# Optimization experiments

Hardware: AMD Instinct MI355X
Metric: run time of the kernel (lower is better)

## Reference

```python
import jax, jax.numpy as jnp
import numpy as np

N_NODES = 50000
N_EDGES = 600000
D = 128


def setup_inputs() -> dict:
    key = jax.random.key(0)
    k = jax.random.split(key, 6)
    x = jax.random.normal(k[0], (N_NODES, D), dtype=jnp.float32)
    edge_src = jax.random.randint(k[1], (N_EDGES,), 0, N_NODES, dtype=jnp.int64 if jax.config.jax_enable_x64 else jnp.int32)
    edge_dst = jax.random.randint(k[2], (N_EDGES,), 0, N_NODES, dtype=jnp.int64 if jax.config.jax_enable_x64 else jnp.int32)
    # message MLP: [h_src ; h_dst] (2D) -> D, update MLP: [h ; agg] (2D) -> D
    scale = 1.0 / np.sqrt(2 * D)
    W1 = jax.random.normal(k[3], (2 * D, D), dtype=jnp.float32) * scale
    b1 = jnp.zeros((D,), dtype=jnp.float32)
    W2 = jax.random.normal(k[4], (2 * D, D), dtype=jnp.float32) * scale
    b2 = jnp.zeros((D,), dtype=jnp.float32)
    return {"x": x, "edge_src": edge_src, "edge_dst": edge_dst,
            "W1": W1, "b1": b1, "W2": W2, "b2": b2}


def reference(x, edge_src, edge_dst, W1, b1, W2, b2):
    # gather endpoint features per edge: [E, 2D]
    pair = jnp.concatenate([x[edge_src], x[edge_dst]], axis=-1)
    # per-edge message MLP: [E, D]
    msg = jax.nn.relu(pair @ W1 + b1)
    # scatter-aggregate (sum) messages into destination nodes: [N, D]
    agg = jax.ops.segment_sum(msg, edge_dst, num_segments=N_NODES)
    # node update MLP with residual: [N, D]
    upd = jax.nn.relu(jnp.concatenate([x, agg], axis=-1) @ W2 + b2)
    return x + upd
```

## Files before the change

### kernel.cpp

```cpp
#include <hip/hip_runtime.h>
#include <stdint.h>


typedef __attribute__((ext_vector_type(8))) short short8;
typedef __attribute__((ext_vector_type(4))) float floatx4;

#define D 128
#define CAP 96

static __device__ __forceinline__ unsigned short f2bf(float f) {
    union { float f; unsigned int u; } v; v.f = f;
    unsigned int r = (v.u + 0x7fffu + ((v.u >> 16) & 1u)) >> 16;
    return (unsigned short)r;
}
static __device__ __forceinline__ float bflo(unsigned int u) {
    union { unsigned int u; float f; } v; v.u = u << 16; return v.f;
}
static __device__ __forceinline__ float bfhi(unsigned int u) {
    union { unsigned int u; float f; } v; v.u = u & 0xffff0000u; return v.f;
}

__global__ void k_pre(const float* __restrict__ W1, const float* __restrict__ W2,
                      unsigned short* __restrict__ w1f, unsigned short* __restrict__ w2f,
                      int* __restrict__ cnt, int N) {
    int gid = blockIdx.x * blockDim.x + threadIdx.x;
    if (gid < (N >> 2)) ((int4*)cnt)[gid] = make_int4(0, 0, 0, 0);
    if (gid < 32768) {
        int tid = gid;
        int j = tid & 7, lane = (tid >> 3) & 63, ct = (tid >> 9) & 15, kk = tid >> 13;
        int k = kk * 32 + (lane >> 4) * 8 + j;
        int c = ((ct >> 2) << 6) + ((lane & 15) << 2) + (ct & 3);
        float v = (c < 128) ? W1[k * 128 + c] : W1[(128 + k) * 128 + (c - 128)];
        w1f[tid] = f2bf(v);
    } else {
        int tid = gid - 32768;
        int j = tid & 7, lane = (tid >> 3) & 63, ct = (tid >> 9) & 7, kk = tid >> 12;
        int k = kk * 32 + (lane >> 4) * 8 + j;
        int c = ((ct >> 1) << 5) + ((lane & 15) << 1) + (ct & 1);
        w2f[tid] = f2bf(W2[k * 128 + c]);
    }
}

__global__ __launch_bounds__(256, 4) void k_fat1(
    const float* __restrict__ x,
    const unsigned short* __restrict__ w1f,
    const float* __restrict__ b1,
    unsigned short* __restrict__ Ys,
    unsigned short* __restrict__ Yd,
    const int* __restrict__ esrc,
    const int* __restrict__ edst,
    int* __restrict__ cnt,
    int* __restrict__ slot,
    int N, int nTiles, int nb1, int E)
{
    const int tid = threadIdx.x;
    if ((int)blockIdx.x >= nb1) {
        const int hthreads = (gridDim.x - nb1) * 256;
        const int hid = (blockIdx.x - nb1) * 256 + tid;
        const int E4 = E >> 2;
        for (int i = hid; i < E4; i += hthreads) {
            int4 s4 = ((const int4*)esrc)[i];
            int4 d4 = ((const int4*)edst)[i];
            int p;
            p = atomicAdd(&cnt[d4.x], 1); if (p < CAP) slot[d4.x * CAP + p] = s4.x;
            p = atomicAdd(&cnt[d4.y], 1); if (p < CAP) slot[d4.y * CAP + p] = s4.y;
            p = atomicAdd(&cnt[d4.z], 1); if (p < CAP) slot[d4.z * CAP + p] = s4.z;
            p = atomicAdd(&cnt[d4.w], 1); if (p < CAP) slot[d4.w * CAP + p] = s4.w;
        }
        for (int i = (E4 << 2) + hid; i < E; i += hthreads) {
            int p = atomicAdd(&cnt[edst[i]], 1);
            if (p < CAP) slot[edst[i] * CAP + p] = esrc[i];
        }
        return;
    }
    const int w = tid >> 6, lane = tid & 63;
    const int quad = lane >> 4, col = lane & 15;

    short8 wf[4][4];
#pragma unroll
    for (int kk = 0; kk < 4; kk++)
#pragma unroll
        for (int j = 0; j < 4; j++)
            wf[kk][j] = ((const short8*)w1f)[(kk * 16 + w * 4 + j) * 64 + lane];
    float4 bias = make_float4(0.f, 0.f, 0.f, 0.f);
    if (w >= 2) bias = *(const float4*)(b1 + (w - 2) * 64 + col * 4);
    unsigned short* Yhalf = (w < 2) ? Ys : Yd;
    const int cb = (w & 1) * 64;

    for (int t = blockIdx.x; t < nTiles; t += nb1) {
        const int n0 = t * 16;
        const int nr = n0 + col;
        const float* xrow = x + (long)nr * D;
        float4 f[8];
#pragma unroll
        for (int kk = 0; kk < 4; kk++) {
            f[kk * 2]     = *(const float4*)(xrow + kk * 32 + quad * 8);
            f[kk * 2 + 1] = *(const float4*)(xrow + kk * 32 + quad * 8 + 4);
        }
        floatx4 acc[4];
#pragma unroll
        for (int j = 0; j < 4; j++)
#pragma unroll
            for (int q = 0; q < 4; q++) acc[j][q] = 0.f;
#pragma unroll
        for (int kk = 0; kk < 4; kk++) {
            union { short8 s; unsigned int u[4]; } au;
            asm("v_cvt_pk_bf16_f32 %0, %1, %2" : "=v"(au.u[0]) : "v"(f[kk*2].x),   "v"(f[kk*2].y));
            asm("v_cvt_pk_bf16_f32 %0, %1, %2" : "=v"(au.u[1]) : "v"(f[kk*2].z),   "v"(f[kk*2].w));
            asm("v_cvt_pk_bf16_f32 %0, %1, %2" : "=v"(au.u[2]) : "v"(f[kk*2+1].x), "v"(f[kk*2+1].y));
            asm("v_cvt_pk_bf16_f32 %0, %1, %2" : "=v"(au.u[3]) : "v"(f[kk*2+1].z), "v"(f[kk*2+1].w));
#pragma unroll
            for (int j = 0; j < 4; j++)
                acc[j] = __builtin_amdgcn_mfma_f32_16x16x32_bf16(au.s, wf[kk][j], acc[j], 0, 0, 0);
        }
#pragma unroll
        for (int r = 0; r < 4; r++) {
            int n = n0 + quad * 4 + r;
            ushort4 o;
            o.x = f2bf(acc[0][r] + bias.x);
            o.y = f2bf(acc[1][r] + bias.y);
            o.z = f2bf(acc[2][r] + bias.z);
            o.w = f2bf(acc[3][r] + bias.w);
            *(ushort4*)(Yhalf + (long)n * D + cb + col * 4) = o;
        }
    }
}

__global__ __launch_bounds__(256) void k_agg(
    const unsigned short* __restrict__ Ys,
    const unsigned short* __restrict__ Yd,
    const int* __restrict__ cnt,
    const int* __restrict__ slot,
    unsigned short* __restrict__ aggb, int N)
{
    int wv = blockIdx.x * 4 + (threadIdx.x >> 6);
    if (wv >= N) return;
    int lane = threadIdx.x & 63;
    int deg = cnt[wv]; if (deg > CAP) deg = CAP;
    const int* sl = slot + wv * CAP;
    unsigned int ydu = *(const unsigned int*)(Yd + (long)wv * D + lane * 2);
    float yd0 = bflo(ydu), yd1 = bfhi(ydu);
    float a0 = 0.f, a1 = 0.f;
    const unsigned short* ysl = Ys + lane * 2;
    int e = 0;
    for (; e + 8 <= deg; e += 8) {
        int s[8]; unsigned int u[8];
#pragma unroll
        for (int q = 0; q < 8; q++) s[q] = sl[e + q];
#pragma unroll
        for (int q = 0; q < 8; q++) u[q] = *(const unsigned int*)(ysl + (long)s[q] * D);
#pragma unroll
        for (int q = 0; q < 8; q++) {
            a0 += fmaxf(bflo(u[q]) + yd0, 0.f);
            a1 += fmaxf(bfhi(u[q]) + yd1, 0.f);
        }
    }
    for (; e + 4 <= deg; e += 4) {
        int s[4]; unsigned int u[4];
#pragma unroll
        for (int q = 0; q < 4; q++) s[q] = sl[e + q];
#pragma unroll
        for (int q = 0; q < 4; q++) u[q] = *(const unsigned int*)(ysl + (long)s[q] * D);
#pragma unroll
        for (int q = 0; q < 4; q++) {
            a0 += fmaxf(bflo(u[q]) + yd0, 0.f);
            a1 += fmaxf(bfhi(u[q]) + yd1, 0.f);
        }
    }
    for (; e < deg; e++) {
        unsigned int u0 = *(const unsigned int*)(ysl + (long)sl[e] * D);
        a0 += fmaxf(bflo(u0) + yd0, 0.f);
        a1 += fmaxf(bfhi(u0) + yd1, 0.f);
    }
    unsigned int o = (unsigned int)f2bf(a0) | ((unsigned int)f2bf(a1) << 16);
    *(unsigned int*)(aggb + (long)wv * D + lane * 2) = o;
}

__global__ __launch_bounds__(256, 4) void k_gemm2(
    const float* __restrict__ x,
    const unsigned short* __restrict__ aggb,
    const unsigned short* __restrict__ w2f,
    const float* __restrict__ b2,
    float* __restrict__ out,
    int N, int nTiles)
{
    const int tid = threadIdx.x, w = tid >> 6, lane = tid & 63;
    const int quad = lane >> 4, col = lane & 15;

    short8 wf[8][2];
#pragma unroll
    for (int kk = 0; kk < 8; kk++)
#pragma unroll
        for (int c = 0; c < 2; c++)
            wf[kk][c] = ((const short8*)w2f)[(kk * 8 + w * 2 + c) * 64 + lane];
    float2 bias = *(const float2*)(b2 + w * 32 + col * 2);

    for (int t = blockIdx.x; t < nTiles; t += gridDim.x) {
        const int n0 = t * 16;
        const int nr = n0 + col;
        const float* xrow = x + (long)nr * D;
        float4 f[8];
        short8 ag[4];
#pragma unroll
        for (int kk = 0; kk < 4; kk++) {
            f[kk * 2]     = *(const float4*)(xrow + kk * 32 + quad * 8);
            f[kk * 2 + 1] = *(const float4*)(xrow + kk * 32 + quad * 8 + 4);
        }
#pragma unroll
        for (int kk = 0; kk < 4; kk++)
            ag[kk] = *(const short8*)(aggb + (long)nr * D + kk * 32 + quad * 8);
        floatx4 acc[2];
#pragma unroll
        for (int c = 0; c < 2; c++)
#pragma unroll
            for (int q = 0; q < 4; q++) acc[c][q] = 0.f;
#pragma unroll
        for (int kk = 0; kk < 4; kk++) {
            union { short8 s; unsigned int u[4]; } au;
            asm("v_cvt_pk_bf16_f32 %0, %1, %2" : "=v"(au.u[0]) : "v"(f[kk*2].x),   "v"(f[kk*2].y));
            asm("v_cvt_pk_bf16_f32 %0, %1, %2" : "=v"(au.u[1]) : "v"(f[kk*2].z),   "v"(f[kk*2].w));
            asm("v_cvt_pk_bf16_f32 %0, %1, %2" : "=v"(au.u[2]) : "v"(f[kk*2+1].x), "v"(f[kk*2+1].y));
            asm("v_cvt_pk_bf16_f32 %0, %1, %2" : "=v"(au.u[3]) : "v"(f[kk*2+1].z), "v"(f[kk*2+1].w));
            acc[0] = __builtin_amdgcn_mfma_f32_16x16x32_bf16(au.s, wf[kk][0], acc[0], 0, 0, 0);
            acc[1] = __builtin_amdgcn_mfma_f32_16x16x32_bf16(au.s, wf[kk][1], acc[1], 0, 0, 0);
        }
#pragma unroll
        for (int kk = 4; kk < 8; kk++) {
            acc[0] = __builtin_amdgcn_mfma_f32_16x16x32_bf16(ag[kk - 4], wf[kk][0], acc[0], 0, 0, 0);
            acc[1] = __builtin_amdgcn_mfma_f32_16x16x32_bf16(ag[kk - 4], wf[kk][1], acc[1], 0, 0, 0);
        }
#pragma unroll
        for (int r = 0; r < 4; r++) {
            int n = n0 + quad * 4 + r;
            long off = (long)n * D + w * 32 + col * 2;
            float2 xr = *(const float2*)(x + off);
            float v0 = fmaxf(acc[0][r] + bias.x, 0.f);
            float v1 = fmaxf(acc[1][r] + bias.y, 0.f);
            *(float2*)(out + off) = make_float2(xr.x + v0, xr.y + v1);
        }
    }
}

extern "C" void kernel_launch(void* const* d_in, const int* in_sizes, int n_in,
                              void* d_out, int out_size, void* d_ws, size_t ws_size,
                              hipStream_t stream)
{
    const float* x   = (const float*)d_in[0];
    const int* esrc  = (const int*)d_in[1];
    const int* edst  = (const int*)d_in[2];
    const float* W1  = (const float*)d_in[3];
    const float* b1  = (const float*)d_in[4];
    const float* W2  = (const float*)d_in[5];
    const float* b2  = (const float*)d_in[6];
    float* out = (float*)d_out;

    const int ND = in_sizes[0];
    const int N  = ND / D;
    const int E  = in_sizes[1];

    char* p = (char*)d_ws;
    auto alloc = [&](size_t bytes) { char* r = p; p += (bytes + 255) & ~(size_t)255; return r; };
    unsigned short* Ys   = (unsigned short*)alloc((size_t)ND * 2);
    unsigned short* Yd   = (unsigned short*)alloc((size_t)ND * 2);
    unsigned short* aggb = (unsigned short*)alloc((size_t)ND * 2);
    unsigned short* w1f  = (unsigned short*)alloc(32768 * 2);
    unsigned short* w2f  = (unsigned short*)alloc(32768 * 2);
    int* cnt  = (int*)alloc((size_t)N * 4);
    int* slot = (int*)alloc((size_t)N * CAP * 4);

    const int nTiles = N / 16;
    const int nb1 = (nTiles + 2) / 3;
    const int nbA = ((E >> 2) + 255) / 256;

    k_pre<<<256, 256, 0, stream>>>(W1, W2, w1f, w2f, cnt, N);
    k_fat1<<<nb1 + nbA, 256, 0, stream>>>(x, w1f, b1, Ys, Yd, esrc, edst, cnt, slot,
                                          N, nTiles, nb1, E);
    k_agg<<<(N + 3) / 4, 256, 0, stream>>>(Ys, Yd, cnt, slot, aggb, N);
    k_gemm2<<<nb1, 256, 0, stream>>>(x, aggb, w2f, b2, out, N, nTiles);
}
```

Baseline: 195.6 us.

## Shard destination buckets eightfold with 16-bit source indices and merge in LDS

```diff
diff --git a/kernel.cpp b/kernel.cpp
--- a/kernel.cpp
+++ b/kernel.cpp
@@ -6,7 +6,7 @@
 typedef __attribute__((ext_vector_type(4))) float floatx4;
 
 #define D 128
-#define CAP 96
+#define CAP8 24
 
 static __device__ __forceinline__ unsigned short f2bf(float f) {
     union { float f; unsigned int u; } v; v.f = f;
@@ -22,9 +22,9 @@
 
 __global__ void k_pre(const float* __restrict__ W1, const float* __restrict__ W2,
                       unsigned short* __restrict__ w1f, unsigned short* __restrict__ w2f,
-                      int* __restrict__ cnt, int N) {
+                      int* __restrict__ cnt8, int N) {
     int gid = blockIdx.x * blockDim.x + threadIdx.x;
-    if (gid < (N >> 2)) ((int4*)cnt)[gid] = make_int4(0, 0, 0, 0);
+    if (gid < 2 * N) ((int4*)cnt8)[gid] = make_int4(0, 0, 0, 0);
     if (gid < 32768) {
         int tid = gid;
         int j = tid & 7, lane = (tid >> 3) & 63, ct = (tid >> 9) & 15, kk = tid >> 13;
@@ -32,7 +32,7 @@
         int c = ((ct >> 2) << 6) + ((lane & 15) << 2) + (ct & 3);
         float v = (c < 128) ? W1[k * 128 + c] : W1[(128 + k) * 128 + (c - 128)];
         w1f[tid] = f2bf(v);
-    } else {
+    } else if (gid < 65536) {
         int tid = gid - 32768;
         int j = tid & 7, lane = (tid >> 3) & 63, ct = (tid >> 9) & 7, kk = tid >> 12;
         int k = kk * 32 + (lane >> 4) * 8 + j;
@@ -49,27 +49,30 @@
     unsigned short* __restrict__ Yd,
     const int* __restrict__ esrc,
     const int* __restrict__ edst,
-    int* __restrict__ cnt,
-    int* __restrict__ slot,
+    int* __restrict__ cnt8,
+    unsigned short* __restrict__ slot16,
     int N, int nTiles, int nb1, int E)
 {
     const int tid = threadIdx.x;
     if ((int)blockIdx.x >= nb1) {
         const int hthreads = (gridDim.x - nb1) * 256;
         const int hid = (blockIdx.x - nb1) * 256 + tid;
+        const int s = blockIdx.x & 7;
+        int* cs = cnt8 + s * N;
+        unsigned short* ss = slot16 + (long)s * N * CAP8;
         const int E4 = E >> 2;
         for (int i = hid; i < E4; i += hthreads) {
             int4 s4 = ((const int4*)esrc)[i];
             int4 d4 = ((const int4*)edst)[i];
             int p;
-            p = atomicAdd(&cnt[d4.x], 1); if (p < CAP) slot[d4.x * CAP + p] = s4.x;
-            p = atomicAdd(&cnt[d4.y], 1); if (p < CAP) slot[d4.y * CAP + p] = s4.y;
-            p = atomicAdd(&cnt[d4.z], 1); if (p < CAP) slot[d4.z * CAP + p] = s4.z;
-            p = atomicAdd(&cnt[d4.w], 1); if (p < CAP) slot[d4.w * CAP + p] = s4.w;
+            p = atomicAdd(&cs[d4.x], 1); if (p < CAP8) ss[d4.x * CAP8 + p] = (unsigned short)s4.x;
+            p = atomicAdd(&cs[d4.y], 1); if (p < CAP8) ss[d4.y * CAP8 + p] = (unsigned short)s4.y;
+            p = atomicAdd(&cs[d4.z], 1); if (p < CAP8) ss[d4.z * CAP8 + p] = (unsigned short)s4.z;
+            p = atomicAdd(&cs[d4.w], 1); if (p < CAP8) ss[d4.w * CAP8 + p] = (unsigned short)s4.w;
         }
         for (int i = (E4 << 2) + hid; i < E; i += hthreads) {
-            int p = atomicAdd(&cnt[edst[i]], 1);
-            if (p < CAP) slot[edst[i] * CAP + p] = esrc[i];
+            int p = atomicAdd(&cs[edst[i]], 1);
+            if (p < CAP8) ss[edst[i] * CAP8 + p] = (unsigned short)esrc[i];
         }
         return;
     }
@@ -129,24 +132,45 @@
 __global__ __launch_bounds__(256) void k_agg(
     const unsigned short* __restrict__ Ys,
     const unsigned short* __restrict__ Yd,
-    const int* __restrict__ cnt,
-    const int* __restrict__ slot,
+    const int* __restrict__ cnt8,
+    const unsigned short* __restrict__ slot16,
     unsigned short* __restrict__ aggb, int N)
 {
-    int wv = blockIdx.x * 4 + (threadIdx.x >> 6);
-    if (wv >= N) return;
-    int lane = threadIdx.x & 63;
-    int deg = cnt[wv]; if (deg > CAP) deg = CAP;
-    const int* sl = slot + wv * CAP;
-    unsigned int ydu = *(const unsigned int*)(Yd + (long)wv * D + lane * 2);
+    __shared__ unsigned short lst[4][8 * CAP8];
+    const int w = threadIdx.x >> 6, lane = threadIdx.x & 63;
+    const int wv = blockIdx.x * 4 + w;
+    const bool act = (wv < N);
+    int deg = 0;
+    if (act) {
+        int ds = 0;
+        if (lane < 8) {
+            ds = cnt8[lane * N + wv];
+            if (ds > CAP8) ds = CAP8;
+        }
+        int run = ds;
+#pragma unroll
+        for (int off = 1; off < 8; off <<= 1) {
+            int t = __shfl_up(run, off, 64);
+            if (lane >= off) run += t;
+        }
+        deg = __shfl(run, 7, 64);
+        if (lane < 8) {
+            int off_s = run - ds;
+            const unsigned short* sp = slot16 + ((long)lane * N + wv) * CAP8;
+            for (int j = 0; j < ds; j++) lst[w][off_s + j] = sp[j];
+        }
+    }
+    __syncthreads();
+    unsigned int ydu = act ? *(const unsigned int*)(Yd + (long)wv * D + lane * 2) : 0u;
     float yd0 = bflo(ydu), yd1 = bfhi(ydu);
     float a0 = 0.f, a1 = 0.f;
     const unsigned short* ysl = Ys + lane * 2;
+    const unsigned short* L = lst[w];
     int e = 0;
     for (; e + 8 <= deg; e += 8) {
         int s[8]; unsigned int u[8];
 #pragma unroll
-        for (int q = 0; q < 8; q++) s[q] = sl[e + q];
+        for (int q = 0; q < 8; q++) s[q] = L[e + q];
 #pragma unroll
         for (int q = 0; q < 8; q++) u[q] = *(const unsigned int*)(ysl + (long)s[q] * D);
 #pragma unroll
@@ -158,7 +182,7 @@
     for (; e + 4 <= deg; e += 4) {
         int s[4]; unsigned int u[4];
 #pragma unroll
-        for (int q = 0; q < 4; q++) s[q] = sl[e + q];
+        for (int q = 0; q < 4; q++) s[q] = L[e + q];
 #pragma unroll
         for (int q = 0; q < 4; q++) u[q] = *(const unsigned int*)(ysl + (long)s[q] * D);
 #pragma unroll
@@ -168,12 +192,14 @@
         }
     }
     for (; e < deg; e++) {
-        unsigned int u0 = *(const unsigned int*)(ysl + (long)sl[e] * D);
+        unsigned int u0 = *(const unsigned int*)(ysl + (long)L[e] * D);
         a0 += fmaxf(bflo(u0) + yd0, 0.f);
         a1 += fmaxf(bfhi(u0) + yd1, 0.f);
     }
-    unsigned int o = (unsigned int)f2bf(a0) | ((unsigned int)f2bf(a1) << 16);
-    *(unsigned int*)(aggb + (long)wv * D + lane * 2) = o;
+    if (act) {
+        unsigned int o = (unsigned int)f2bf(a0) | ((unsigned int)f2bf(a1) << 16);
+        *(unsigned int*)(aggb + (long)wv * D + lane * 2) = o;
+    }
 }
 
 __global__ __launch_bounds__(256, 4) void k_gemm2(
@@ -260,21 +286,22 @@
 
     char* p = (char*)d_ws;
     auto alloc = [&](size_t bytes) { char* r = p; p += (bytes + 255) & ~(size_t)255; return r; };
-    unsigned short* Ys   = (unsigned short*)alloc((size_t)ND * 2);
-    unsigned short* Yd   = (unsigned short*)alloc((size_t)ND * 2);
-    unsigned short* aggb = (unsigned short*)alloc((size_t)ND * 2);
-    unsigned short* w1f  = (unsigned short*)alloc(32768 * 2);
-    unsigned short* w2f  = (unsigned short*)alloc(32768 * 2);
-    int* cnt  = (int*)alloc((size_t)N * 4);
-    int* slot = (int*)alloc((size_t)N * CAP * 4);
+    unsigned short* Ys     = (unsigned short*)alloc((size_t)ND * 2);
+    unsigned short* Yd     = (unsigned short*)alloc((size_t)ND * 2);
+    unsigned short* aggb   = (unsigned short*)alloc((size_t)ND * 2);
+    unsigned short* w1f    = (unsigned short*)alloc(32768 * 2);
+    unsigned short* w2f    = (unsigned short*)alloc(32768 * 2);
+    int* cnt8              = (int*)alloc((size_t)8 * N * 4);
+    unsigned short* slot16 = (unsigned short*)alloc((size_t)8 * N * CAP8 * 2);
 
     const int nTiles = N / 16;
     const int nb1 = (nTiles + 2) / 3;
     const int nbA = ((E >> 2) + 255) / 256;
-
-    k_pre<<<256, 256, 0, stream>>>(W1, W2, w1f, w2f, cnt, N);
-    k_fat1<<<nb1 + nbA, 256, 0, stream>>>(x, w1f, b1, Ys, Yd, esrc, edst, cnt, slot,
+    const int preThreads = (2 * N > 65536) ? 2 * N : 65536;
+
+    k_pre<<<(preThreads + 255) / 256, 256, 0, stream>>>(W1, W2, w1f, w2f, cnt8, N);
+    k_fat1<<<nb1 + nbA, 256, 0, stream>>>(x, w1f, b1, Ys, Yd, esrc, edst, cnt8, slot16,
                                           N, nTiles, nb1, E);
-    k_agg<<<(N + 3) / 4, 256, 0, stream>>>(Ys, Yd, cnt, slot, aggb, N);
+    k_agg<<<(N + 3) / 4, 256, 0, stream>>>(Ys, Yd, cnt8, slot16, aggb, N);
     k_gemm2<<<nb1, 256, 0, stream>>>(x, aggb, w2f, b2, out, N, nTiles);
 }
```

Result: faster. 191.3 us (-2.2%).

## Bucket edges by 64-node destination blocks and aggregate in shared memory

Applied to the files above, without the earlier changes.

```diff
diff --git a/kernel.cpp b/kernel.cpp
--- a/kernel.cpp
+++ b/kernel.cpp
@@ -6,7 +6,9 @@
 typedef __attribute__((ext_vector_type(4))) float floatx4;
 
 #define D 128
-#define CAP 96
+#define BSH 6
+#define BNODES 64
+#define BCAP 1024
 
 static __device__ __forceinline__ unsigned short f2bf(float f) {
     union { float f; unsigned int u; } v; v.f = f;
@@ -22,9 +24,10 @@
 
 __global__ void k_pre(const float* __restrict__ W1, const float* __restrict__ W2,
                       unsigned short* __restrict__ w1f, unsigned short* __restrict__ w2f,
-                      int* __restrict__ cnt, int N) {
+                      int* __restrict__ bcnt, int N) {
     int gid = blockIdx.x * blockDim.x + threadIdx.x;
-    if (gid < (N >> 2)) ((int4*)cnt)[gid] = make_int4(0, 0, 0, 0);
+    int nb16 = (((N + BNODES - 1) >> BSH) << 4);
+    if (gid < nb16) bcnt[gid] = 0;
     if (gid < 32768) {
         int tid = gid;
         int j = tid & 7, lane = (tid >> 3) & 63, ct = (tid >> 9) & 15, kk = tid >> 13;
@@ -32,7 +35,7 @@
         int c = ((ct >> 2) << 6) + ((lane & 15) << 2) + (ct & 3);
         float v = (c < 128) ? W1[k * 128 + c] : W1[(128 + k) * 128 + (c - 128)];
         w1f[tid] = f2bf(v);
-    } else {
+    } else if (gid < 65536) {
         int tid = gid - 32768;
         int j = tid & 7, lane = (tid >> 3) & 63, ct = (tid >> 9) & 7, kk = tid >> 12;
         int k = kk * 32 + (lane >> 4) * 8 + j;
@@ -49,8 +52,8 @@
     unsigned short* __restrict__ Yd,
     const int* __restrict__ esrc,
     const int* __restrict__ edst,
-    int* __restrict__ cnt,
-    int* __restrict__ slot,
+    int* __restrict__ bcnt,
+    unsigned int* __restrict__ bslot,
     int N, int nTiles, int nb1, int E)
 {
     const int tid = threadIdx.x;
@@ -62,14 +65,24 @@
             int4 s4 = ((const int4*)esrc)[i];
             int4 d4 = ((const int4*)edst)[i];
             int p;
-            p = atomicAdd(&cnt[d4.x], 1); if (p < CAP) slot[d4.x * CAP + p] = s4.x;
-            p = atomicAdd(&cnt[d4.y], 1); if (p < CAP) slot[d4.y * CAP + p] = s4.y;
-            p = atomicAdd(&cnt[d4.z], 1); if (p < CAP) slot[d4.z * CAP + p] = s4.z;
-            p = atomicAdd(&cnt[d4.w], 1); if (p < CAP) slot[d4.w * CAP + p] = s4.w;
+            p = atomicAdd(&bcnt[(d4.x >> BSH) << 4], 1);
+            if (p < BCAP) bslot[((long)(d4.x >> BSH) << 10) + p] =
+                ((unsigned int)(d4.x & (BNODES - 1)) << 16) | (unsigned int)s4.x;
+            p = atomicAdd(&bcnt[(d4.y >> BSH) << 4], 1);
+            if (p < BCAP) bslot[((long)(d4.y >> BSH) << 10) + p] =
+                ((unsigned int)(d4.y & (BNODES - 1)) << 16) | (unsigned int)s4.y;
+            p = atomicAdd(&bcnt[(d4.z >> BSH) << 4], 1);
+            if (p < BCAP) bslot[((long)(d4.z >> BSH) << 10) + p] =
+                ((unsigned int)(d4.z & (BNODES - 1)) << 16) | (unsigned int)s4.z;
+            p = atomicAdd(&bcnt[(d4.w >> BSH) << 4], 1);
+            if (p < BCAP) bslot[((long)(d4.w >> BSH) << 10) + p] =
+                ((unsigned int)(d4.w & (BNODES - 1)) << 16) | (unsigned int)s4.w;
         }
         for (int i = (E4 << 2) + hid; i < E; i += hthreads) {
-            int p = atomicAdd(&cnt[edst[i]], 1);
-            if (p < CAP) slot[edst[i] * CAP + p] = esrc[i];
+            int d = edst[i];
+            int p = atomicAdd(&bcnt[(d >> BSH) << 4], 1);
+            if (p < BCAP) bslot[((long)(d >> BSH) << 10) + p] =
+                ((unsigned int)(d & (BNODES - 1)) << 16) | (unsigned int)esrc[i];
         }
         return;
     }
@@ -126,54 +139,77 @@
     }
 }
 
-__global__ __launch_bounds__(256) void k_agg(
+__global__ __launch_bounds__(256, 3) void k_agg(
     const unsigned short* __restrict__ Ys,
     const unsigned short* __restrict__ Yd,
-    const int* __restrict__ cnt,
-    const int* __restrict__ slot,
+    const int* __restrict__ bcnt,
+    const unsigned int* __restrict__ bslot,
     unsigned short* __restrict__ aggb, int N)
 {
-    int wv = blockIdx.x * 4 + (threadIdx.x >> 6);
-    if (wv >= N) return;
-    int lane = threadIdx.x & 63;
-    int deg = cnt[wv]; if (deg > CAP) deg = CAP;
-    const int* sl = slot + wv * CAP;
-    unsigned int ydu = *(const unsigned int*)(Yd + (long)wv * D + lane * 2);
-    float yd0 = bflo(ydu), yd1 = bfhi(ydu);
-    float a0 = 0.f, a1 = 0.f;
+    __shared__ float acc[BNODES * D];
+    __shared__ unsigned int ydl[BNODES * (D / 2)];
+    const int tid = threadIdx.x, w = tid >> 6, lane = tid & 63;
+    const int b = blockIdx.x;
+    const int nb0 = b << BSH;
+    int nd = N - nb0; if (nd > BNODES) nd = BNODES;
+
+#pragma unroll
+    for (int i = 0; i < (BNODES * D) / 256; i++)
+        acc[tid + i * 256] = 0.f;
+    for (int i = tid; i < nd * (D / 2); i += 256) {
+        int row = i >> 6, colu = i & 63;
+        ydl[i] = *(const unsigned int*)(Yd + (long)(nb0 + row) * D + colu * 2);
+    }
+    __syncthreads();
+
+    int bc = bcnt[b << 4]; if (bc > BCAP) bc = BCAP;
+    const unsigned int* slots = bslot + ((long)b << 10);
     const unsigned short* ysl = Ys + lane * 2;
-    int e = 0;
-    for (; e + 8 <= deg; e += 8) {
-        int s[8]; unsigned int u[8];
-#pragma unroll
-        for (int q = 0; q < 8; q++) s[q] = sl[e + q];
-#pragma unroll
-        for (int q = 0; q < 8; q++) u[q] = *(const unsigned int*)(ysl + (long)s[q] * D);
-#pragma unroll
-        for (int q = 0; q < 8; q++) {
-            a0 += fmaxf(bflo(u[q]) + yd0, 0.f);
-            a1 += fmaxf(bfhi(u[q]) + yd1, 0.f);
-        }
-    }
-    for (; e + 4 <= deg; e += 4) {
-        int s[4]; unsigned int u[4];
-#pragma unroll
-        for (int q = 0; q < 4; q++) s[q] = sl[e + q];
-#pragma unroll
-        for (int q = 0; q < 4; q++) u[q] = *(const unsigned int*)(ysl + (long)s[q] * D);
-#pragma unroll
-        for (int q = 0; q < 4; q++) {
-            a0 += fmaxf(bflo(u[q]) + yd0, 0.f);
-            a1 += fmaxf(bfhi(u[q]) + yd1, 0.f);
-        }
-    }
-    for (; e < deg; e++) {
-        unsigned int u0 = *(const unsigned int*)(ysl + (long)sl[e] * D);
-        a0 += fmaxf(bflo(u0) + yd0, 0.f);
-        a1 += fmaxf(bfhi(u0) + yd1, 0.f);
-    }
-    unsigned int o = (unsigned int)f2bf(a0) | ((unsigned int)f2bf(a1) << 16);
-    *(unsigned int*)(aggb + (long)wv * D + lane * 2) = o;
+
+    for (int c0 = w << 6; c0 < bc; c0 += 256) {
+        int nj = bc - c0; if (nj > 64) nj = 64;
+        unsigned int myp = (lane < nj) ? slots[c0 + lane] : 0u;
+        int j = 0;
+        for (; j + 4 <= nj; j += 4) {
+            unsigned int p0 = __shfl(myp, j, 64);
+            unsigned int p1 = __shfl(myp, j + 1, 64);
+            unsigned int p2 = __shfl(myp, j + 2, 64);
+            unsigned int p3 = __shfl(myp, j + 3, 64);
+            unsigned int u0 = *(const unsigned int*)(ysl + (long)(p0 & 0xffffu) * D);
+            unsigned int u1 = *(const unsigned int*)(ysl + (long)(p1 & 0xffffu) * D);
+            unsigned int u2 = *(const unsigned int*)(ysl + (long)(p2 & 0xffffu) * D);
+            unsigned int u3 = *(const unsigned int*)(ysl + (long)(p3 & 0xffffu) * D);
+            int d0 = p0 >> 16, d1 = p1 >> 16, d2 = p2 >> 16, d3 = p3 >> 16;
+            unsigned int y0 = ydl[(d0 << 6) + lane];
+            unsigned int y1 = ydl[(d1 << 6) + lane];
+            unsigned int y2 = ydl[(d2 << 6) + lane];
+            unsigned int y3 = ydl[(d3 << 6) + lane];
+            atomicAdd(&acc[(d0 << 7) + lane * 2],     fmaxf(bflo(u0) + bflo(y0), 0.f));
+            atomicAdd(&acc[(d0 << 7) + lane * 2 + 1], fmaxf(bfhi(u0) + bfhi(y0), 0.f));
+            atomicAdd(&acc[(d1 << 7) + lane * 2],     fmaxf(bflo(u1) + bflo(y1), 0.f));
+            atomicAdd(&acc[(d1 << 7) + lane * 2 + 1], fmaxf(bfhi(u1) + bfhi(y1), 0.f));
+            atomicAdd(&acc[(d2 << 7) + lane * 2],     fmaxf(bflo(u2) + bflo(y2), 0.f));
+            atomicAdd(&acc[(d2 << 7) + lane * 2 + 1], fmaxf(bfhi(u2) + bfhi(y2), 0.f));
+            atomicAdd(&acc[(d3 << 7) + lane * 2],     fmaxf(bflo(u3) + bflo(y3), 0.f));
+            atomicAdd(&acc[(d3 << 7) + lane * 2 + 1], fmaxf(bfhi(u3) + bfhi(y3), 0.f));
+        }
+        for (; j < nj; j++) {
+            unsigned int p0 = __shfl(myp, j, 64);
+            unsigned int u0 = *(const unsigned int*)(ysl + (long)(p0 & 0xffffu) * D);
+            int d0 = p0 >> 16;
+            unsigned int y0 = ydl[(d0 << 6) + lane];
+            atomicAdd(&acc[(d0 << 7) + lane * 2],     fmaxf(bflo(u0) + bflo(y0), 0.f));
+            atomicAdd(&acc[(d0 << 7) + lane * 2 + 1], fmaxf(bfhi(u0) + bfhi(y0), 0.f));
+        }
+    }
+    __syncthreads();
+    for (int i = tid; i < nd * (D / 2); i += 256) {
+        int row = i >> 6, colu = i & 63;
+        float a0 = acc[(row << 7) + colu * 2];
+        float a1 = acc[(row << 7) + colu * 2 + 1];
+        unsigned int o = (unsigned int)f2bf(a0) | ((unsigned int)f2bf(a1) << 16);
+        *(unsigned int*)(aggb + (long)(nb0 + row) * D + colu * 2) = o;
+    }
 }
 
 __global__ __launch_bounds__(256, 4) void k_gemm2(
@@ -265,16 +301,18 @@
     unsigned short* aggb = (unsigned short*)alloc((size_t)ND * 2);
     unsigned short* w1f  = (unsigned short*)alloc(32768 * 2);
     unsigned short* w2f  = (unsigned short*)alloc(32768 * 2);
-    int* cnt  = (int*)alloc((size_t)N * 4);
-    int* slot = (int*)alloc((size_t)N * CAP * 4);
+
+    const int NB = (N + BNODES - 1) >> BSH;
+    int* bcnt          = (int*)alloc((size_t)NB * 16 * 4);
+    unsigned int* bslot = (unsigned int*)alloc((size_t)NB * BCAP * 4);
 
     const int nTiles = N / 16;
     const int nb1 = (nTiles + 2) / 3;
     const int nbA = ((E >> 2) + 255) / 256;
 
-    k_pre<<<256, 256, 0, stream>>>(W1, W2, w1f, w2f, cnt, N);
-    k_fat1<<<nb1 + nbA, 256, 0, stream>>>(x, w1f, b1, Ys, Yd, esrc, edst, cnt, slot,
+    k_pre<<<256, 256, 0, stream>>>(W1, W2, w1f, w2f, bcnt, N);
+    k_fat1<<<nb1 + nbA, 256, 0, stream>>>(x, w1f, b1, Ys, Yd, esrc, edst, bcnt, bslot,
                                           N, nTiles, nb1, E);
-    k_agg<<<(N + 3) / 4, 256, 0, stream>>>(Ys, Yd, cnt, slot, aggb, N);
+    k_agg<<<NB, 256, 0, stream>>>(Ys, Yd, bcnt, bslot, aggb, N);
     k_gemm2<<<nb1, 256, 0, stream>>>(x, aggb, w2f, b2, out, N, nTiles);
 }
```

Measured after the change: 683.2 us. 3.49x slower.

## Bucket edges by 64-node destination blocks and sort per block in shared memory

Applied to the files above, without the earlier changes.

```diff
diff --git a/kernel.cpp b/kernel.cpp
--- a/kernel.cpp
+++ b/kernel.cpp
@@ -6,7 +6,9 @@
 typedef __attribute__((ext_vector_type(4))) float floatx4;
 
 #define D 128
-#define CAP 96
+#define BSH 6
+#define BNODES 64
+#define BCAP 1024
 
 static __device__ __forceinline__ unsigned short f2bf(float f) {
     union { float f; unsigned int u; } v; v.f = f;
@@ -22,9 +24,10 @@
 
 __global__ void k_pre(const float* __restrict__ W1, const float* __restrict__ W2,
                       unsigned short* __restrict__ w1f, unsigned short* __restrict__ w2f,
-                      int* __restrict__ cnt, int N) {
+                      int* __restrict__ bcnt, int N) {
     int gid = blockIdx.x * blockDim.x + threadIdx.x;
-    if (gid < (N >> 2)) ((int4*)cnt)[gid] = make_int4(0, 0, 0, 0);
+    int nb16 = (((N + BNODES - 1) >> BSH) << 4);
+    if (gid < nb16) bcnt[gid] = 0;
     if (gid < 32768) {
         int tid = gid;
         int j = tid & 7, lane = (tid >> 3) & 63, ct = (tid >> 9) & 15, kk = tid >> 13;
@@ -32,7 +35,7 @@
         int c = ((ct >> 2) << 6) + ((lane & 15) << 2) + (ct & 3);
         float v = (c < 128) ? W1[k * 128 + c] : W1[(128 + k) * 128 + (c - 128)];
         w1f[tid] = f2bf(v);
-    } else {
+    } else if (gid < 65536) {
         int tid = gid - 32768;
         int j = tid & 7, lane = (tid >> 3) & 63, ct = (tid >> 9) & 7, kk = tid >> 12;
         int k = kk * 32 + (lane >> 4) * 8 + j;
@@ -49,8 +52,8 @@
     unsigned short* __restrict__ Yd,
     const int* __restrict__ esrc,
     const int* __restrict__ edst,
-    int* __restrict__ cnt,
-    int* __restrict__ slot,
+    int* __restrict__ bcnt,
+    unsigned int* __restrict__ bslot,
     int N, int nTiles, int nb1, int E)
 {
     const int tid = threadIdx.x;
@@ -62,14 +65,24 @@
             int4 s4 = ((const int4*)esrc)[i];
             int4 d4 = ((const int4*)edst)[i];
             int p;
-            p = atomicAdd(&cnt[d4.x], 1); if (p < CAP) slot[d4.x * CAP + p] = s4.x;
-            p = atomicAdd(&cnt[d4.y], 1); if (p < CAP) slot[d4.y * CAP + p] = s4.y;
-            p = atomicAdd(&cnt[d4.z], 1); if (p < CAP) slot[d4.z * CAP + p] = s4.z;
-            p = atomicAdd(&cnt[d4.w], 1); if (p < CAP) slot[d4.w * CAP + p] = s4.w;
+            p = atomicAdd(&bcnt[(d4.x >> BSH) << 4], 1);
+            if (p < BCAP) bslot[((long)(d4.x >> BSH) << 10) + p] =
+                ((unsigned int)(d4.x & (BNODES - 1)) << 16) | (unsigned int)s4.x;
+            p = atomicAdd(&bcnt[(d4.y >> BSH) << 4], 1);
+            if (p < BCAP) bslot[((long)(d4.y >> BSH) << 10) + p] =
+                ((unsigned int)(d4.y & (BNODES - 1)) << 16) | (unsigned int)s4.y;
+            p = atomicAdd(&bcnt[(d4.z >> BSH) << 4], 1);
+            if (p < BCAP) bslot[((long)(d4.z >> BSH) << 10) + p] =
+                ((unsigned int)(d4.z & (BNODES - 1)) << 16) | (unsigned int)s4.z;
+            p = atomicAdd(&bcnt[(d4.w >> BSH) << 4], 1);
+            if (p < BCAP) bslot[((long)(d4.w >> BSH) << 10) + p] =
+                ((unsigned int)(d4.w & (BNODES - 1)) << 16) | (unsigned int)s4.w;
         }
         for (int i = (E4 << 2) + hid; i < E; i += hthreads) {
-            int p = atomicAdd(&cnt[edst[i]], 1);
-            if (p < CAP) slot[edst[i] * CAP + p] = esrc[i];
+            int d = edst[i];
+            int p = atomicAdd(&bcnt[(d >> BSH) << 4], 1);
+            if (p < BCAP) bslot[((long)(d >> BSH) << 10) + p] =
+                ((unsigned int)(d & (BNODES - 1)) << 16) | (unsigned int)esrc[i];
         }
         return;
     }
@@ -126,54 +139,91 @@
     }
 }
 
-__global__ __launch_bounds__(256) void k_agg(
+__global__ __launch_bounds__(512, 2) void k_agg(
     const unsigned short* __restrict__ Ys,
     const unsigned short* __restrict__ Yd,
-    const int* __restrict__ cnt,
-    const int* __restrict__ slot,
+    const int* __restrict__ bcnt,
+    const unsigned int* __restrict__ bslot,
     unsigned short* __restrict__ aggb, int N)
 {
-    int wv = blockIdx.x * 4 + (threadIdx.x >> 6);
-    if (wv >= N) return;
-    int lane = threadIdx.x & 63;
-    int deg = cnt[wv]; if (deg > CAP) deg = CAP;
-    const int* sl = slot + wv * CAP;
-    unsigned int ydu = *(const unsigned int*)(Yd + (long)wv * D + lane * 2);
-    float yd0 = bflo(ydu), yd1 = bfhi(ydu);
-    float a0 = 0.f, a1 = 0.f;
+    __shared__ unsigned int eb[BCAP];
+    __shared__ unsigned short sorted[BCAP];
+    __shared__ int cnt64[BNODES], start64[BNODES], cur64[BNODES];
+    const int tid = threadIdx.x, w = tid >> 6, lane = tid & 63;
+    const int b = blockIdx.x, nb0 = b << BSH;
+    int nd = N - nb0; if (nd > BNODES) nd = BNODES;
+    int bc = bcnt[b << 4]; if (bc > BCAP) bc = BCAP;
+
+    if (tid < BNODES) cnt64[tid] = 0;
+    __syncthreads();
+    for (int i = tid; i < bc; i += 512) {
+        unsigned int e = bslot[((long)b << 10) + i];
+        eb[i] = e;
+        atomicAdd(&cnt64[e >> 16], 1);
+    }
+    __syncthreads();
+    if (tid < 64) {
+        int c = cnt64[tid];
+        int incl = c;
+#pragma unroll
+        for (int off = 1; off < 64; off <<= 1) {
+            int t = __shfl_up(incl, off, 64);
+            if (lane >= off) incl += t;
+        }
+        start64[tid] = incl - c;
+        cur64[tid] = incl - c;
+    }
+    __syncthreads();
+    for (int i = tid; i < bc; i += 512) {
+        unsigned int e = eb[i];
+        int p = atomicAdd(&cur64[e >> 16], 1);
+        sorted[p] = (unsigned short)(e & 0xffffu);
+    }
+    __syncthreads();
+
     const unsigned short* ysl = Ys + lane * 2;
-    int e = 0;
-    for (; e + 8 <= deg; e += 8) {
-        int s[8]; unsigned int u[8];
-#pragma unroll
-        for (int q = 0; q < 8; q++) s[q] = sl[e + q];
-#pragma unroll
-        for (int q = 0; q < 8; q++) u[q] = *(const unsigned int*)(ysl + (long)s[q] * D);
-#pragma unroll
-        for (int q = 0; q < 8; q++) {
-            a0 += fmaxf(bflo(u[q]) + yd0, 0.f);
-            a1 += fmaxf(bfhi(u[q]) + yd1, 0.f);
-        }
-    }
-    for (; e + 4 <= deg; e += 4) {
-        int s[4]; unsigned int u[4];
-#pragma unroll
-        for (int q = 0; q < 4; q++) s[q] = sl[e + q];
-#pragma unroll
-        for (int q = 0; q < 4; q++) u[q] = *(const unsigned int*)(ysl + (long)s[q] * D);
-#pragma unroll
-        for (int q = 0; q < 4; q++) {
-            a0 += fmaxf(bflo(u[q]) + yd0, 0.f);
-            a1 += fmaxf(bfhi(u[q]) + yd1, 0.f);
-        }
-    }
-    for (; e < deg; e++) {
-        unsigned int u0 = *(const unsigned int*)(ysl + (long)sl[e] * D);
-        a0 += fmaxf(bflo(u0) + yd0, 0.f);
-        a1 += fmaxf(bfhi(u0) + yd1, 0.f);
-    }
-    unsigned int o = (unsigned int)f2bf(a0) | ((unsigned int)f2bf(a1) << 16);
-    *(unsigned int*)(aggb + (long)wv * D + lane * 2) = o;
+#pragma unroll
+    for (int k = 0; k < 8; k++) {
+        int ln = w * 8 + k;
+        if (ln >= nd) break;
+        const int node = nb0 + ln;
+        const int deg = cnt64[ln], base = start64[ln];
+        unsigned int ydu = *(const unsigned int*)(Yd + (long)node * D + lane * 2);
+        float yd0 = bflo(ydu), yd1 = bfhi(ydu);
+        float a0 = 0.f, a1 = 0.f;
+        int e = 0;
+        for (; e + 8 <= deg; e += 8) {
+            int s[8]; unsigned int u[8];
+#pragma unroll
+            for (int q = 0; q < 8; q++) s[q] = sorted[base + e + q];
+#pragma unroll
+            for (int q = 0; q < 8; q++) u[q] = *(const unsigned int*)(ysl + (long)s[q] * D);
+#pragma unroll
+            for (int q = 0; q < 8; q++) {
+                a0 += fmaxf(bflo(u[q]) + yd0, 0.f);
+                a1 += fmaxf(bfhi(u[q]) + yd1, 0.f);
+            }
+        }
+        for (; e + 4 <= deg; e += 4) {
+            int s[4]; unsigned int u[4];
+#pragma unroll
+            for (int q = 0; q < 4; q++) s[q] = sorted[base + e + q];
+#pragma unroll
+            for (int q = 0; q < 4; q++) u[q] = *(const unsigned int*)(ysl + (long)s[q] * D);
+#pragma unroll
+            for (int q = 0; q < 4; q++) {
+                a0 += fmaxf(bflo(u[q]) + yd0, 0.f);
+                a1 += fmaxf(bfhi(u[q]) + yd1, 0.f);
+            }
+        }
+        for (; e < deg; e++) {
+            unsigned int u0 = *(const unsigned int*)(ysl + (long)sorted[base + e] * D);
+            a0 += fmaxf(bflo(u0) + yd0, 0.f);
+            a1 += fmaxf(bfhi(u0) + yd1, 0.f);
+        }
+        unsigned int o = (unsigned int)f2bf(a0) | ((unsigned int)f2bf(a1) << 16);
+        *(unsigned int*)(aggb + (long)node * D + lane * 2) = o;
+    }
 }
 
 __global__ __launch_bounds__(256, 4) void k_gemm2(
@@ -265,16 +315,18 @@
     unsigned short* aggb = (unsigned short*)alloc((size_t)ND * 2);
     unsigned short* w1f  = (unsigned short*)alloc(32768 * 2);
     unsigned short* w2f  = (unsigned short*)alloc(32768 * 2);
-    int* cnt  = (int*)alloc((size_t)N * 4);
-    int* slot = (int*)alloc((size_t)N * CAP * 4);
+
+    const int NB = (N + BNODES - 1) >> BSH;
+    int* bcnt           = (int*)alloc((size_t)NB * 16 * 4);
+    unsigned int* bslot = (unsigned int*)alloc((size_t)NB * BCAP * 4);
 
     const int nTiles = N / 16;
     const int nb1 = (nTiles + 2) / 3;
     const int nbA = ((E >> 2) + 255) / 256;
 
-    k_pre<<<256, 256, 0, stream>>>(W1, W2, w1f, w2f, cnt, N);
-    k_fat1<<<nb1 + nbA, 256, 0, stream>>>(x, w1f, b1, Ys, Yd, esrc, edst, cnt, slot,
+    k_pre<<<256, 256, 0, stream>>>(W1, W2, w1f, w2f, bcnt, N);
+    k_fat1<<<nb1 + nbA, 256, 0, stream>>>(x, w1f, b1, Ys, Yd, esrc, edst, bcnt, bslot,
                                           N, nTiles, nb1, E);
-    k_agg<<<(N + 3) / 4, 256, 0, stream>>>(Ys, Yd, cnt, slot, aggb, N);
+    k_agg<<<NB, 512, 0, stream>>>(Ys, Yd, bcnt, bslot, aggb, N);
     k_gemm2<<<nb1, 256, 0, stream>>>(x, aggb, w2f, b2, out, N, nTiles);
 }
```

New measurement: 185.6 us. -5.1%, faster.
